# Performance work log

Measured on AMD Instinct MI355X. Metric: run time of the kernel, lower is better.

## Reference

```python
import jax, jax.numpy as jnp
import numpy as np


def setup_inputs() -> dict:
    key = jax.random.key(0)
    k1, k2, k3 = jax.random.split(key, 3)
    B, T, N = 256, 512, 128
    logits = jax.random.normal(k1, (B, T, N), dtype=jnp.float32)
    transitions = jax.random.normal(k2, (N, N), dtype=jnp.float32) * 0.1
    sequence_lengths = jax.random.randint(k3, (B,), 1, T + 1, dtype=jnp.int32)
    return {"logits": logits, "transitions": transitions,
            "sequence_lengths": sequence_lengths}


def reference(logits, transitions, sequence_lengths):
    # Viterbi decode (tfa.text.crf.crf_decode) + sequence mask, as in CRF.call.
    B, T, N = logits.shape
    state0 = logits[:, 0, :]                                  # [B,N]
    xs = jnp.moveaxis(logits[:, 1:, :], 1, 0)                 # [T-1,B,N]
    # step i (time t=i+1) is active iff t < seq_len
    active = jnp.arange(1, T)[:, None] < sequence_lengths[None, :]  # [T-1,B]

    def fwd_step(state, inp):
        x_t, act = inp
        # max-plus update: scores[b,i,j] = state[b,i] + transitions[i,j]
        scores = state[:, :, None] + transitions[None, :, :]  # [B,N,N]
        bp = jnp.argmax(scores, axis=1).astype(jnp.int32)     # [B,N]
        new_state = jnp.max(scores, axis=1) + x_t             # [B,N]
        # freeze state past the end of each sequence
        state = jnp.where(act[:, None], new_state, state)
        return state, bp

    final_state, bps = jax.lax.scan(fwd_step, state0, (xs, active))
    last_tag = jnp.argmax(final_state, axis=-1).astype(jnp.int32)  # [B]

    def bwd_step(cur, inp):
        bp_t, act = inp
        new = jnp.take_along_axis(bp_t, cur[:, None], axis=1)[:, 0]
        cur = jnp.where(act, new, cur)
        return cur, cur

    # reverse scan: ys[t] = decoded tag at time t, for t = 0..T-2
    _, tags = jax.lax.scan(bwd_step, last_tag, (bps, active), reverse=True)
    pred_ids = jnp.concatenate([jnp.moveaxis(tags, 0, 1),
                                last_tag[:, None]], axis=1)   # [B,T]
    mask = (jnp.arange(T)[None, :] < sequence_lengths[:, None]).astype(pred_ids.dtype)
    return pred_ids * mask
```

## Files before the change

kernel.cpp:

```cpp
#include <hip/hip_runtime.h>

#define TT 512
#define NN 128
#define NTHR 512
#define SROW 160
#define SW(i) (20 * ((i) >> 4) + ((i) & 15))
#define TTS 130
#define BD  64
#define MAXG 8

#define STEP_BARRIER() asm volatile("s_waitcnt lgkmcnt(0)\n\ts_barrier" ::: "memory")

template <int CTRL>
__device__ __forceinline__ int dpp_i(int x) {
    return __builtin_amdgcn_update_dpp(x, x, CTRL, 0xf, 0xf, true);
}
template <int CTRL>
__device__ __forceinline__ float dpp_f(float x) {
    union { float f; int i; } u; u.f = x;
    u.i = dpp_i<CTRL>(u.i);
    return u.f;
}
#define DPP_XOR1 0xB1
#define DPP_XOR2 0x4E
#define DPP_MIR7 0x141

__global__ __launch_bounds__(NTHR, 1)
void crf_viterbi_fast(const float* __restrict__ logits,
                      const float* __restrict__ trans,
                      const int* __restrict__ seqlen,
                      int* __restrict__ out,
                      float* __restrict__ ws) {
    __shared__ float stateBuf[2][SROW];
    __shared__ float tt[NN * TTS];
    __shared__ float redV[NN];
    __shared__ int   redI[NN];
    __shared__ int   tagBuf[TT];

    const int tid = threadIdx.x;
    const int j   = tid >> 3;
    const int c   = tid & 7;
    const int i0  = c << 4;
    const int b   = blockIdx.x;
    const int L   = seqlen[b];
    const int lm1 = L - 1;
    const int jx  = j + ((c & 1) << 6);

    const float* lrow = logits + (size_t)b * TT * NN;
    float* wsb = ws + (size_t)b * TT * NN;

    auto xl = [&](int r) -> float {
        r = (r < lm1) ? r : lm1;
        return lrow[r * NN + jx];
    };
    float X0 = xl(1), X1 = xl(2), X2 = xl(3), X3 = xl(4);

    float tr0[16], tr1[16];
    #pragma unroll
    for (int k = 0; k < 16; ++k) {
        tr0[k] = trans[(i0 + k) * NN + j];
        tr1[k] = trans[(i0 + k) * NN + j + 64];
    }

    #pragma unroll
    for (int k = 0; k < (NN * NN) / NTHR; ++k) {
        int idx = k * NTHR + tid;
        tt[(idx & 127) * TTS + (idx >> 7)] = trans[idx];
    }

    if (c < 2) {
        stateBuf[0][SW(jx)] = lrow[jx];
        wsb[jx] = 0.0f;
    }
    __syncthreads();

    #define TAGMAX(TR, OUT)                                                    \
    {                                                                          \
        float c0=a0.x+TR[0], c1=a0.y+TR[1], c2=a0.z+TR[2],  c3=a0.w+TR[3];     \
        float c4=a1.x+TR[4], c5=a1.y+TR[5], c6=a1.z+TR[6],  c7=a1.w+TR[7];     \
        float c8=a2.x+TR[8], c9=a2.y+TR[9], c10=a2.z+TR[10],c11=a2.w+TR[11];   \
        float c12=a3.x+TR[12],c13=a3.y+TR[13],c14=a3.z+TR[14],c15=a3.w+TR[15]; \
        float t0=fmaxf(fmaxf(c0,c1),c2),  t1=fmaxf(fmaxf(c3,c4),c5);           \
        float t2=fmaxf(fmaxf(c6,c7),c8),  t3=fmaxf(fmaxf(c9,c10),c11);         \
        float t4=fmaxf(fmaxf(c12,c13),c14);                                    \
        OUT = fmaxf(fmaxf(fmaxf(t0,t1),t2), fmaxf(fmaxf(t3,t4),c15));          \
    }

    auto vstep = [&](const float* st, float* dst, int t, float& xslot) {
        float xa_use = xslot;
        int tn = t + 4;
        tn = (tn < lm1) ? tn : lm1;
        xslot = lrow[tn * NN + jx];

        const float* sp = st + 20 * c;
        float4 a0 = *(const float4*)(sp);
        float4 a1 = *(const float4*)(sp + 4);
        float4 a2 = *(const float4*)(sp + 8);
        float4 a3 = *(const float4*)(sp + 12);

        float bv0, bv1;
        TAGMAX(tr0, bv0)
        TAGMAX(tr1, bv1)

        bv0 = fmaxf(bv0, dpp_f<DPP_XOR1>(bv0)); bv1 = fmaxf(bv1, dpp_f<DPP_XOR1>(bv1));
        bv0 = fmaxf(bv0, dpp_f<DPP_XOR2>(bv0)); bv1 = fmaxf(bv1, dpp_f<DPP_XOR2>(bv1));
        bv0 = fmaxf(bv0, dpp_f<DPP_MIR7>(bv0)); bv1 = fmaxf(bv1, dpp_f<DPP_MIR7>(bv1));

        if (c < 2) {
            float bv = c ? bv1 : bv0;
            dst[SW(jx)] = bv + xa_use;
            wsb[t * NN + jx] = bv;
        }
        STEP_BARRIER();
    };
    #undef TAGMAX

    int t = 1;
    for (; t + 4 < L; t += 4) {
        vstep(stateBuf[0], stateBuf[1], t,     X0);
        vstep(stateBuf[1], stateBuf[0], t + 1, X1);
        vstep(stateBuf[0], stateBuf[1], t + 2, X2);
        vstep(stateBuf[1], stateBuf[0], t + 3, X3);
    }
    if (t     < L) vstep(stateBuf[0], stateBuf[1], t,     X0);
    if (t + 1 < L) vstep(stateBuf[1], stateBuf[0], t + 1, X1);
    if (t + 2 < L) vstep(stateBuf[0], stateBuf[1], t + 2, X2);
    if (t + 3 < L) vstep(stateBuf[1], stateBuf[0], t + 3, X3);

    __syncthreads();
    const int pf = (L - 1) & 1;

    if (tid < NN) { redV[tid] = stateBuf[pf][SW(tid)]; redI[tid] = tid; }
    __syncthreads();
    #pragma unroll
    for (int off = 64; off >= 1; off >>= 1) {
        if (tid < off) {
            float va = redV[tid], vb = redV[tid + off];
            int   ia = redI[tid], ib = redI[tid + off];
            if (vb > va || (vb == va && ib < ia)) { redV[tid] = vb; redI[tid] = ib; }
        }
        __syncthreads();
    }

    if (tid < 64) {
        const int lane = tid;
        int jc = redI[0];
        if (lane == 0) tagBuf[L - 1] = jc;

        auto wrow = [&](int r) -> float2 {
            r = (r < 0) ? 0 : r;
            return *(const float2*)(wsb + r * NN + 2 * lane);
        };
        auto xrow = [&](int r) -> float2 {
            r = (r < 0) ? 0 : r;
            return *(const float2*)(lrow + r * NN + 2 * lane);
        };
        auto extract2 = [&](float2 v, int idx) -> float {
            int sel = idx >> 1;
            int wx = __builtin_amdgcn_readlane(__float_as_int(v.x), sel);
            int wy = __builtin_amdgcn_readlane(__float_as_int(v.y), sel);
            return __int_as_float((idx & 1) ? wy : wx);
        };

        float target;
        {
            float2 rT = wrow(L - 1);
            target = extract2(rT, jc);
        }

        auto chase = [&](float2 m, float2 xr, int tc) {
            float2 tp = *(const float2*)(tt + jc * TTS + 2 * lane);
            float cA = (m.x + xr.x) + tp.x;
            float cB = (m.y + xr.y) + tp.y;
            unsigned long long mA = __ballot(cA == target);
            unsigned long long mB = __ballot(cB == target);
            int iA = mA ? (2 * (__ffsll(mA) - 1))     : (1 << 30);
            int iB = mB ? (2 * (__ffsll(mB) - 1) + 1) : (1 << 30);
            int bp = (iA < iB) ? iA : iB;
            if (lane == 0) tagBuf[tc - 1] = bp;
            target = extract2(m, bp);
            jc = bp;
        };

        float2 m0 = wrow(L - 2), x0 = xrow(L - 2);
        float2 m1 = wrow(L - 3), x1 = xrow(L - 3);
        float2 m2 = wrow(L - 4), x2 = xrow(L - 4);
        float2 m3 = wrow(L - 5), x3 = xrow(L - 5);
        float2 m4 = wrow(L - 6), x4 = xrow(L - 6);
        float2 m5 = wrow(L - 7), x5 = xrow(L - 7);
        float2 m6 = wrow(L - 8), x6 = xrow(L - 8);
        float2 m7 = wrow(L - 9), x7 = xrow(L - 9);
        int tb = L - 1;
        while (tb >= 8) {
            chase(m0, x0, tb);     m0 = wrow(tb - 9);  x0 = xrow(tb - 9);
            chase(m1, x1, tb - 1); m1 = wrow(tb - 10); x1 = xrow(tb - 10);
            chase(m2, x2, tb - 2); m2 = wrow(tb - 11); x2 = xrow(tb - 11);
            chase(m3, x3, tb - 3); m3 = wrow(tb - 12); x3 = xrow(tb - 12);
            chase(m4, x4, tb - 4); m4 = wrow(tb - 13); x4 = xrow(tb - 13);
            chase(m5, x5, tb - 5); m5 = wrow(tb - 14); x5 = xrow(tb - 14);
            chase(m6, x6, tb - 6); m6 = wrow(tb - 15); x6 = xrow(tb - 15);
            chase(m7, x7, tb - 7); m7 = wrow(tb - 16); x7 = xrow(tb - 16);
            tb -= 8;
        }
        if (tb >= 1) chase(m0, x0, tb);
        if (tb >= 2) chase(m1, x1, tb - 1);
        if (tb >= 3) chase(m2, x2, tb - 2);
        if (tb >= 4) chase(m3, x3, tb - 3);
        if (tb >= 5) chase(m4, x4, tb - 4);
        if (tb >= 6) chase(m5, x5, tb - 5);
        if (tb >= 7) chase(m6, x6, tb - 6);
    }
    __syncthreads();

    out[(size_t)b * TT + tid] = (tid < L) ? tagBuf[tid] : 0;
}

__global__ __launch_bounds__(NTHR, 1)
void crf_viterbi_fallback(const float* __restrict__ logits,
                          const float* __restrict__ trans,
                          const int* __restrict__ seqlen,
                          int* __restrict__ out) {
    __shared__ float stateBuf[2][SROW];
    __shared__ float redV[NN];
    __shared__ int   redI[NN];
    __shared__ int   tagBuf[TT];
    __shared__ int   entryTag[MAXG];
    __shared__ unsigned char bp[TT][NN];
    __shared__ unsigned char hist[MAXG][BD][NN];

    const int tid = threadIdx.x;
    const int j   = tid >> 3;
    const int c   = tid & 7;
    const int i0  = c << 4;
    const int b   = blockIdx.x;
    const int L   = seqlen[b];

    float tr0[16], tr1[16];
    #pragma unroll
    for (int k = 0; k < 16; ++k) {
        tr0[k] = trans[(i0 + k) * NN + j];
        tr1[k] = trans[(i0 + k) * NN + j + 64];
    }

    const float* lrow = logits + (size_t)b * TT * NN;
    if (c < 2) {
        int jj = j + (c << 6);
        stateBuf[0][SW(jj)] = lrow[jj];
    }
    __syncthreads();

    float xa0 = lrow[NN + j], xa1 = lrow[NN + j + 64];
    int p = 0;
    for (int t = 1; t < L; ++t) {
        int tn = (t + 1 < L) ? (t + 1) : (L - 1);
        const float* lp = lrow + tn * NN;
        float xb0 = lp[j];
        float xb1 = lp[j + 64];

        const float* st = stateBuf[p] + 20 * c;
        float4 a0 = *(const float4*)(st);
        float4 a1 = *(const float4*)(st + 4);
        float4 a2 = *(const float4*)(st + 8);
        float4 a3 = *(const float4*)(st + 12);

        float best0 = -__builtin_inff(), best1 = -__builtin_inff();
        int arg0 = 0, arg1 = 0;
        #define ELEM(S, K)                                                  \
        {                                                                   \
            float sc = (S) + tr0[K];                                        \
            bool g = sc > best0; best0 = g ? sc : best0; arg0 = g ? (K) : arg0; \
            float sd = (S) + tr1[K];                                        \
            bool h = sd > best1; best1 = h ? sd : best1; arg1 = h ? (K) : arg1; \
        }
        ELEM(a0.x, 0)  ELEM(a0.y, 1)  ELEM(a0.z, 2)  ELEM(a0.w, 3)
        ELEM(a1.x, 4)  ELEM(a1.y, 5)  ELEM(a1.z, 6)  ELEM(a1.w, 7)
        ELEM(a2.x, 8)  ELEM(a2.y, 9)  ELEM(a2.z, 10) ELEM(a2.w, 11)
        ELEM(a3.x, 12) ELEM(a3.y, 13) ELEM(a3.z, 14) ELEM(a3.w, 15)
        #undef ELEM

        float bv0 = best0, bv1 = best1;
        int   bi0 = i0 + arg0, bi1 = i0 + arg1;
        #define MERGE_STAGE(CTRL, LOWER)                                   \
        {                                                                  \
            float p0 = dpp_f<CTRL>(bv0); int q0 = dpp_i<CTRL>(bi0);        \
            float p1 = dpp_f<CTRL>(bv1); int q1 = dpp_i<CTRL>(bi1);        \
            bool lower = (LOWER);                                          \
            bool t0 = (p0 > bv0) || (p0 == bv0 && lower);                  \
            bool t1 = (p1 > bv1) || (p1 == bv1 && lower);                  \
            bv0 = t0 ? p0 : bv0; bi0 = t0 ? q0 : bi0;                      \
            bv1 = t1 ? p1 : bv1; bi1 = t1 ? q1 : bi1;                      \
        }
        MERGE_STAGE(DPP_XOR1, (c & 1) != 0)
        MERGE_STAGE(DPP_XOR2, (c & 2) != 0)
        MERGE_STAGE(DPP_MIR7, (c & 4) != 0)
        #undef MERGE_STAGE

        if (c < 2) {
            int   jj = j + (c << 6);
            float bv = c ? bv1 : bv0;
            int   bi = c ? bi1 : bi0;
            float xx = c ? xa1 : xa0;
            stateBuf[p ^ 1][SW(jj)] = bv + xx;
            bp[t][jj] = (unsigned char)bi;
        }
        xa0 = xb0; xa1 = xb1;
        __syncthreads();
        p ^= 1;
    }

    if (tid < NN) { redV[tid] = stateBuf[p][SW(tid)]; redI[tid] = tid; }
    __syncthreads();
    #pragma unroll
    for (int off = 64; off >= 1; off >>= 1) {
        if (tid < off) {
            float va = redV[tid], vb = redV[tid + off];
            int   ia = redI[tid], ib = redI[tid + off];
            if (vb > va || (vb == va && ib < ia)) { redV[tid] = vb; redI[tid] = ib; }
        }
        __syncthreads();
    }

    const int M = L - 1;
    const int G = (M + BD - 1) / BD;
    {
        int s  = tid & 127;
        int gA = tid >> 7;
        int gB = gA + 4;
        int thA = M - gA * BD, thB = M - gB * BD;
        int dA  = (gA < G) ? ((thA < BD) ? thA : BD) : 0;
        int dB  = (gB < G) ? ((thB < BD) ? thB : BD) : 0;
        int curA = s, curB = s;
        int maxd = (dA > dB) ? dA : dB;
        for (int d = 0; d < maxd; ++d) {
            if (d < dA) { curA = bp[thA - d][curA]; hist[gA][d][s] = (unsigned char)curA; }
            if (d < dB) { curB = bp[thB - d][curB]; hist[gB][d][s] = (unsigned char)curB; }
        }
    }
    __syncthreads();
    if (tid == 0) {
        int e = redI[0];
        tagBuf[L - 1] = e;
        for (int g = 0; g < G; ++g) {
            entryTag[g] = e;
            if (g + 1 < G) e = hist[g][BD - 1][e];
        }
    }
    __syncthreads();
    {
        int g = tid >> 6, d = tid & 63;
        if (g < MAXG && g < G) {
            int th  = M - g * BD;
            int dep = (th < BD) ? th : BD;
            if (d < dep) {
                int e = entryTag[g];
                tagBuf[th - 1 - d] = hist[g][d][e];
            }
        }
    }
    __syncthreads();
    out[(size_t)b * TT + tid] = (tid < L) ? tagBuf[tid] : 0;
}

extern "C" void kernel_launch(void* const* d_in, const int* in_sizes, int n_in,
                              void* d_out, int out_size, void* d_ws, size_t ws_size,
                              hipStream_t stream) {
    const float* logits = (const float*)d_in[0];
    const float* trans  = (const float*)d_in[1];
    const int*   seqlen = (const int*)d_in[2];
    int*         out    = (int*)d_out;
    const int B = in_sizes[2];
    const size_t need = (size_t)B * TT * NN * sizeof(float);
    if (ws_size >= need) {
        crf_viterbi_fast<<<B, NTHR, 0, stream>>>(logits, trans, seqlen, out,
                                                 (float*)d_ws);
    } else {
        crf_viterbi_fallback<<<B, NTHR, 0, stream>>>(logits, trans, seqlen, out);
    }
}
```

Baseline: 313.6 us.

## Store uint8 backpointers in LDS and use parallel block traceback

The forward pass now computes each step's argmax with an equality search against the max, reduced with DPP min, and writes byte backpointers into shared memory. This replaces spilling max values to a global workspace and re-deriving argmaxes in a serial wave-level chase during traceback. The backward pass reuses the fallback kernel's chunked history-composition traceback, and the adds use packed float2 vectors. In exchange, every forward step does extra compare and DPP work and the kernel uses much more LDS.

```diff
diff --git a/kernel.cpp b/kernel.cpp
--- a/kernel.cpp
+++ b/kernel.cpp
@@ -5,11 +5,12 @@
 #define NTHR 512
 #define SROW 160
 #define SW(i) (20 * ((i) >> 4) + ((i) & 15))
-#define TTS 130
 #define BD  64
 #define MAXG 8
 
 #define STEP_BARRIER() asm volatile("s_waitcnt lgkmcnt(0)\n\ts_barrier" ::: "memory")
+
+typedef float v2f __attribute__((ext_vector_type(2)));
 
 template <int CTRL>
 __device__ __forceinline__ int dpp_i(int x) {
@@ -26,16 +27,17 @@
 #define DPP_MIR7 0x141
 
 __global__ __launch_bounds__(NTHR, 1)
-void crf_viterbi_fast(const float* __restrict__ logits,
-                      const float* __restrict__ trans,
-                      const int* __restrict__ seqlen,
-                      int* __restrict__ out,
-                      float* __restrict__ ws) {
+void crf_viterbi(const float* __restrict__ logits,
+                 const float* __restrict__ trans,
+                 const int* __restrict__ seqlen,
+                 int* __restrict__ out) {
     __shared__ float stateBuf[2][SROW];
-    __shared__ float tt[NN * TTS];
     __shared__ float redV[NN];
     __shared__ int   redI[NN];
     __shared__ int   tagBuf[TT];
+    __shared__ int   entryTag[MAXG];
+    __shared__ unsigned char bp[TT][NN];
+    __shared__ unsigned char hist[MAXG][BD][NN];
 
     const int tid = threadIdx.x;
     const int j   = tid >> 3;
@@ -47,7 +49,6 @@
     const int jx  = j + ((c & 1) << 6);
 
     const float* lrow = logits + (size_t)b * TT * NN;
-    float* wsb = ws + (size_t)b * TT * NN;
 
     auto xl = [&](int r) -> float {
         r = (r < lm1) ? r : lm1;
@@ -55,36 +56,17 @@
     };
     float X0 = xl(1), X1 = xl(2), X2 = xl(3), X3 = xl(4);
 
-    float tr0[16], tr1[16];
+    v2f tr0[8], tr1[8];
     #pragma unroll
-    for (int k = 0; k < 16; ++k) {
-        tr0[k] = trans[(i0 + k) * NN + j];
-        tr1[k] = trans[(i0 + k) * NN + j + 64];
-    }
-
-    #pragma unroll
-    for (int k = 0; k < (NN * NN) / NTHR; ++k) {
-        int idx = k * NTHR + tid;
-        tt[(idx & 127) * TTS + (idx >> 7)] = trans[idx];
-    }
-
-    if (c < 2) {
-        stateBuf[0][SW(jx)] = lrow[jx];
-        wsb[jx] = 0.0f;
-    }
-    __syncthreads();
-
-    #define TAGMAX(TR, OUT)                                                    \
-    {                                                                          \
-        float c0=a0.x+TR[0], c1=a0.y+TR[1], c2=a0.z+TR[2],  c3=a0.w+TR[3];     \
-        float c4=a1.x+TR[4], c5=a1.y+TR[5], c6=a1.z+TR[6],  c7=a1.w+TR[7];     \
-        float c8=a2.x+TR[8], c9=a2.y+TR[9], c10=a2.z+TR[10],c11=a2.w+TR[11];   \
-        float c12=a3.x+TR[12],c13=a3.y+TR[13],c14=a3.z+TR[14],c15=a3.w+TR[15]; \
-        float t0=fmaxf(fmaxf(c0,c1),c2),  t1=fmaxf(fmaxf(c3,c4),c5);           \
-        float t2=fmaxf(fmaxf(c6,c7),c8),  t3=fmaxf(fmaxf(c9,c10),c11);         \
-        float t4=fmaxf(fmaxf(c12,c13),c14);                                    \
-        OUT = fmaxf(fmaxf(fmaxf(t0,t1),t2), fmaxf(fmaxf(t3,t4),c15));          \
-    }
+    for (int p = 0; p < 8; ++p) {
+        tr0[p].x = trans[(i0 + 2 * p)     * NN + j];
+        tr0[p].y = trans[(i0 + 2 * p + 1) * NN + j];
+        tr1[p].x = trans[(i0 + 2 * p)     * NN + j + 64];
+        tr1[p].y = trans[(i0 + 2 * p + 1) * NN + j + 64];
+    }
+
+    if (c < 2) stateBuf[0][SW(jx)] = lrow[jx];
+    __syncthreads();
 
     auto vstep = [&](const float* st, float* dst, int t, float& xslot) {
         float xa_use = xslot;
@@ -98,9 +80,34 @@
         float4 a2 = *(const float4*)(sp + 8);
         float4 a3 = *(const float4*)(sp + 12);
 
+        v2f sv0 = {a0.x, a0.y}, sv1 = {a0.z, a0.w};
+        v2f sv2 = {a1.x, a1.y}, sv3 = {a1.z, a1.w};
+        v2f sv4 = {a2.x, a2.y}, sv5 = {a2.z, a2.w};
+        v2f sv6 = {a3.x, a3.y}, sv7 = {a3.z, a3.w};
+
+        v2f cc0[8], cc1[8];
+        cc0[0] = sv0 + tr0[0]; cc1[0] = sv0 + tr1[0];
+        cc0[1] = sv1 + tr0[1]; cc1[1] = sv1 + tr1[1];
+        cc0[2] = sv2 + tr0[2]; cc1[2] = sv2 + tr1[2];
+        cc0[3] = sv3 + tr0[3]; cc1[3] = sv3 + tr1[3];
+        cc0[4] = sv4 + tr0[4]; cc1[4] = sv4 + tr1[4];
+        cc0[5] = sv5 + tr0[5]; cc1[5] = sv5 + tr1[5];
+        cc0[6] = sv6 + tr0[6]; cc1[6] = sv6 + tr1[6];
+        cc0[7] = sv7 + tr0[7]; cc1[7] = sv7 + tr1[7];
+
+        #define TREE(CC, OUT)                                                  \
+        {                                                                      \
+            float t0 = fmaxf(fmaxf(CC[0].x, CC[0].y), CC[1].x);                \
+            float t1 = fmaxf(fmaxf(CC[1].y, CC[2].x), CC[2].y);                \
+            float t2 = fmaxf(fmaxf(CC[3].x, CC[3].y), CC[4].x);                \
+            float t3 = fmaxf(fmaxf(CC[4].y, CC[5].x), CC[5].y);                \
+            float t4 = fmaxf(fmaxf(CC[6].x, CC[6].y), CC[7].x);                \
+            OUT = fmaxf(fmaxf(fmaxf(t0, t1), t2), fmaxf(fmaxf(t3, t4), CC[7].y)); \
+        }
         float bv0, bv1;
-        TAGMAX(tr0, bv0)
-        TAGMAX(tr1, bv1)
+        TREE(cc0, bv0)
+        TREE(cc1, bv1)
+        #undef TREE
 
         bv0 = fmaxf(bv0, dpp_f<DPP_XOR1>(bv0)); bv1 = fmaxf(bv1, dpp_f<DPP_XOR1>(bv1));
         bv0 = fmaxf(bv0, dpp_f<DPP_XOR2>(bv0)); bv1 = fmaxf(bv1, dpp_f<DPP_XOR2>(bv1));
@@ -109,11 +116,26 @@
         if (c < 2) {
             float bv = c ? bv1 : bv0;
             dst[SW(jx)] = bv + xa_use;
-            wsb[t * NN + jx] = bv;
-        }
+        }
+
+        int idx0 = 255, idx1 = 255;
+        #pragma unroll
+        for (int k = 7; k >= 0; --k) {
+            if (cc0[k].y == bv0) idx0 = 2 * k + 1;
+            if (cc1[k].y == bv1) idx1 = 2 * k + 1;
+            if (cc0[k].x == bv0) idx0 = 2 * k;
+            if (cc1[k].x == bv1) idx1 = 2 * k;
+        }
+        int v0 = i0 + idx0;
+        int v1 = i0 + idx1;
+        v0 = min(v0, dpp_i<DPP_XOR1>(v0)); v1 = min(v1, dpp_i<DPP_XOR1>(v1));
+        v0 = min(v0, dpp_i<DPP_XOR2>(v0)); v1 = min(v1, dpp_i<DPP_XOR2>(v1));
+        v0 = min(v0, dpp_i<DPP_MIR7>(v0)); v1 = min(v1, dpp_i<DPP_MIR7>(v1));
+
+        if (c < 2) bp[t][jx] = (unsigned char)(c ? v1 : v0);
+
         STEP_BARRIER();
     };
-    #undef TAGMAX
 
     int t = 1;
     for (; t + 4 < L; t += 4) {
@@ -131,184 +153,6 @@
     const int pf = (L - 1) & 1;
 
     if (tid < NN) { redV[tid] = stateBuf[pf][SW(tid)]; redI[tid] = tid; }
-    __syncthreads();
-    #pragma unroll
-    for (int off = 64; off >= 1; off >>= 1) {
-        if (tid < off) {
-            float va = redV[tid], vb = redV[tid + off];
-            int   ia = redI[tid], ib = redI[tid + off];
-            if (vb > va || (vb == va && ib < ia)) { redV[tid] = vb; redI[tid] = ib; }
-        }
-        __syncthreads();
-    }
-
-    if (tid < 64) {
-        const int lane = tid;
-        int jc = redI[0];
-        if (lane == 0) tagBuf[L - 1] = jc;
-
-        auto wrow = [&](int r) -> float2 {
-            r = (r < 0) ? 0 : r;
-            return *(const float2*)(wsb + r * NN + 2 * lane);
-        };
-        auto xrow = [&](int r) -> float2 {
-            r = (r < 0) ? 0 : r;
-            return *(const float2*)(lrow + r * NN + 2 * lane);
-        };
-        auto extract2 = [&](float2 v, int idx) -> float {
-            int sel = idx >> 1;
-            int wx = __builtin_amdgcn_readlane(__float_as_int(v.x), sel);
-            int wy = __builtin_amdgcn_readlane(__float_as_int(v.y), sel);
-            return __int_as_float((idx & 1) ? wy : wx);
-        };
-
-        float target;
-        {
-            float2 rT = wrow(L - 1);
-            target = extract2(rT, jc);
-        }
-
-        auto chase = [&](float2 m, float2 xr, int tc) {
-            float2 tp = *(const float2*)(tt + jc * TTS + 2 * lane);
-            float cA = (m.x + xr.x) + tp.x;
-            float cB = (m.y + xr.y) + tp.y;
-            unsigned long long mA = __ballot(cA == target);
-            unsigned long long mB = __ballot(cB == target);
-            int iA = mA ? (2 * (__ffsll(mA) - 1))     : (1 << 30);
-            int iB = mB ? (2 * (__ffsll(mB) - 1) + 1) : (1 << 30);
-            int bp = (iA < iB) ? iA : iB;
-            if (lane == 0) tagBuf[tc - 1] = bp;
-            target = extract2(m, bp);
-            jc = bp;
-        };
-
-        float2 m0 = wrow(L - 2), x0 = xrow(L - 2);
-        float2 m1 = wrow(L - 3), x1 = xrow(L - 3);
-        float2 m2 = wrow(L - 4), x2 = xrow(L - 4);
-        float2 m3 = wrow(L - 5), x3 = xrow(L - 5);
-        float2 m4 = wrow(L - 6), x4 = xrow(L - 6);
-        float2 m5 = wrow(L - 7), x5 = xrow(L - 7);
-        float2 m6 = wrow(L - 8), x6 = xrow(L - 8);
-        float2 m7 = wrow(L - 9), x7 = xrow(L - 9);
-        int tb = L - 1;
-        while (tb >= 8) {
-            chase(m0, x0, tb);     m0 = wrow(tb - 9);  x0 = xrow(tb - 9);
-            chase(m1, x1, tb - 1); m1 = wrow(tb - 10); x1 = xrow(tb - 10);
-            chase(m2, x2, tb - 2); m2 = wrow(tb - 11); x2 = xrow(tb - 11);
-            chase(m3, x3, tb - 3); m3 = wrow(tb - 12); x3 = xrow(tb - 12);
-            chase(m4, x4, tb - 4); m4 = wrow(tb - 13); x4 = xrow(tb - 13);
-            chase(m5, x5, tb - 5); m5 = wrow(tb - 14); x5 = xrow(tb - 14);
-            chase(m6, x6, tb - 6); m6 = wrow(tb - 15); x6 = xrow(tb - 15);
-            chase(m7, x7, tb - 7); m7 = wrow(tb - 16); x7 = xrow(tb - 16);
-            tb -= 8;
-        }
-        if (tb >= 1) chase(m0, x0, tb);
-        if (tb >= 2) chase(m1, x1, tb - 1);
-        if (tb >= 3) chase(m2, x2, tb - 2);
-        if (tb >= 4) chase(m3, x3, tb - 3);
-        if (tb >= 5) chase(m4, x4, tb - 4);
-        if (tb >= 6) chase(m5, x5, tb - 5);
-        if (tb >= 7) chase(m6, x6, tb - 6);
-    }
-    __syncthreads();
-
-    out[(size_t)b * TT + tid] = (tid < L) ? tagBuf[tid] : 0;
-}
-
-__global__ __launch_bounds__(NTHR, 1)
-void crf_viterbi_fallback(const float* __restrict__ logits,
-                          const float* __restrict__ trans,
-                          const int* __restrict__ seqlen,
-                          int* __restrict__ out) {
-    __shared__ float stateBuf[2][SROW];
-    __shared__ float redV[NN];
-    __shared__ int   redI[NN];
-    __shared__ int   tagBuf[TT];
-    __shared__ int   entryTag[MAXG];
-    __shared__ unsigned char bp[TT][NN];
-    __shared__ unsigned char hist[MAXG][BD][NN];
-
-    const int tid = threadIdx.x;
-    const int j   = tid >> 3;
-    const int c   = tid & 7;
-    const int i0  = c << 4;
-    const int b   = blockIdx.x;
-    const int L   = seqlen[b];
-
-    float tr0[16], tr1[16];
-    #pragma unroll
-    for (int k = 0; k < 16; ++k) {
-        tr0[k] = trans[(i0 + k) * NN + j];
-        tr1[k] = trans[(i0 + k) * NN + j + 64];
-    }
-
-    const float* lrow = logits + (size_t)b * TT * NN;
-    if (c < 2) {
-        int jj = j + (c << 6);
-        stateBuf[0][SW(jj)] = lrow[jj];
-    }
-    __syncthreads();
-
-    float xa0 = lrow[NN + j], xa1 = lrow[NN + j + 64];
-    int p = 0;
-    for (int t = 1; t < L; ++t) {
-        int tn = (t + 1 < L) ? (t + 1) : (L - 1);
-        const float* lp = lrow + tn * NN;
-        float xb0 = lp[j];
-        float xb1 = lp[j + 64];
-
-        const float* st = stateBuf[p] + 20 * c;
-        float4 a0 = *(const float4*)(st);
-        float4 a1 = *(const float4*)(st + 4);
-        float4 a2 = *(const float4*)(st + 8);
-        float4 a3 = *(const float4*)(st + 12);
-
-        float best0 = -__builtin_inff(), best1 = -__builtin_inff();
-        int arg0 = 0, arg1 = 0;
-        #define ELEM(S, K)                                                  \
-        {                                                                   \
-            float sc = (S) + tr0[K];                                        \
-            bool g = sc > best0; best0 = g ? sc : best0; arg0 = g ? (K) : arg0; \
-            float sd = (S) + tr1[K];                                        \
-            bool h = sd > best1; best1 = h ? sd : best1; arg1 = h ? (K) : arg1; \
-        }
-        ELEM(a0.x, 0)  ELEM(a0.y, 1)  ELEM(a0.z, 2)  ELEM(a0.w, 3)
-        ELEM(a1.x, 4)  ELEM(a1.y, 5)  ELEM(a1.z, 6)  ELEM(a1.w, 7)
-        ELEM(a2.x, 8)  ELEM(a2.y, 9)  ELEM(a2.z, 10) ELEM(a2.w, 11)
-        ELEM(a3.x, 12) ELEM(a3.y, 13) ELEM(a3.z, 14) ELEM(a3.w, 15)
-        #undef ELEM
-
-        float bv0 = best0, bv1 = best1;
-        int   bi0 = i0 + arg0, bi1 = i0 + arg1;
-        #define MERGE_STAGE(CTRL, LOWER)                                   \
-        {                                                                  \
-            float p0 = dpp_f<CTRL>(bv0); int q0 = dpp_i<CTRL>(bi0);        \
-            float p1 = dpp_f<CTRL>(bv1); int q1 = dpp_i<CTRL>(bi1);        \
-            bool lower = (LOWER);                                          \
-            bool t0 = (p0 > bv0) || (p0 == bv0 && lower);                  \
-            bool t1 = (p1 > bv1) || (p1 == bv1 && lower);                  \
-            bv0 = t0 ? p0 : bv0; bi0 = t0 ? q0 : bi0;                      \
-            bv1 = t1 ? p1 : bv1; bi1 = t1 ? q1 : bi1;                      \
-        }
-        MERGE_STAGE(DPP_XOR1, (c & 1) != 0)
-        MERGE_STAGE(DPP_XOR2, (c & 2) != 0)
-        MERGE_STAGE(DPP_MIR7, (c & 4) != 0)
-        #undef MERGE_STAGE
-
-        if (c < 2) {
-            int   jj = j + (c << 6);
-            float bv = c ? bv1 : bv0;
-            int   bi = c ? bi1 : bi0;
-            float xx = c ? xa1 : xa0;
-            stateBuf[p ^ 1][SW(jj)] = bv + xx;
-            bp[t][jj] = (unsigned char)bi;
-        }
-        xa0 = xb0; xa1 = xb1;
-        __syncthreads();
-        p ^= 1;
-    }
-
-    if (tid < NN) { redV[tid] = stateBuf[p][SW(tid)]; redI[tid] = tid; }
     __syncthreads();
     #pragma unroll
     for (int off = 64; off >= 1; off >>= 1) {
@@ -358,6 +202,7 @@
         }
     }
     __syncthreads();
+
     out[(size_t)b * TT + tid] = (tid < L) ? tagBuf[tid] : 0;
 }
 
@@ -369,11 +214,6 @@
     const int*   seqlen = (const int*)d_in[2];
     int*         out    = (int*)d_out;
     const int B = in_sizes[2];
-    const size_t need = (size_t)B * TT * NN * sizeof(float);
-    if (ws_size >= need) {
-        crf_viterbi_fast<<<B, NTHR, 0, stream>>>(logits, trans, seqlen, out,
-                                                 (float*)d_ws);
-    } else {
-        crf_viterbi_fallback<<<B, NTHR, 0, stream>>>(logits, trans, seqlen, out);
-    }
-}
+    (void)d_ws; (void)ws_size;
+    crf_viterbi<<<B, NTHR, 0, stream>>>(logits, trans, seqlen, out);
+}
```

New measurement: 420.2 us. 1.34x slower.

## Halve fast-kernel threads, give each lane 32 states with packed v2f max-plus

Applied to the files above, without the earlier changes.

The fast Viterbi kernel now runs 256 threads instead of 512, so each output tag is reduced by 4 lanes over 32 predecessor states rather than 8 lanes over 16. The inner max-plus reduction is written with 2-wide float vectors so the compiler can emit packed FP32 adds, and one DPP shuffle stage is removed. The aim is to cut per-step barrier cost and cross-lane shuffle latency on the serial time recurrence. In exchange, each lane does twice as much arithmetic per step, needs more registers, and the epilogue writes two outputs per thread. The fallback kernel keeps 512 threads via a separate define.

```diff
diff --git a/kernel.cpp b/kernel.cpp
--- a/kernel.cpp
+++ b/kernel.cpp
@@ -2,7 +2,8 @@
 
 #define TT 512
 #define NN 128
-#define NTHR 512
+#define NTHR 256
+#define FTHR 512
 #define SROW 160
 #define SW(i) (20 * ((i) >> 4) + ((i) & 15))
 #define TTS 130
@@ -10,6 +11,11 @@
 #define MAXG 8
 
 #define STEP_BARRIER() asm volatile("s_waitcnt lgkmcnt(0)\n\ts_barrier" ::: "memory")
+
+typedef float v2f __attribute__((ext_vector_type(2)));
+__device__ __forceinline__ v2f vmax2(v2f a, v2f b) {
+    v2f r; r.x = fmaxf(a.x, b.x); r.y = fmaxf(a.y, b.y); return r;
+}
 
 template <int CTRL>
 __device__ __forceinline__ int dpp_i(int x) {
@@ -38,9 +44,9 @@
     __shared__ int   tagBuf[TT];
 
     const int tid = threadIdx.x;
-    const int j   = tid >> 3;
-    const int c   = tid & 7;
-    const int i0  = c << 4;
+    const int j   = tid >> 2;
+    const int c   = tid & 3;
+    const int i0  = c << 5;
     const int b   = blockIdx.x;
     const int L   = seqlen[b];
     const int lm1 = L - 1;
@@ -55,14 +61,15 @@
     };
     float X0 = xl(1), X1 = xl(2), X2 = xl(3), X3 = xl(4);
 
-    float tr0[16], tr1[16];
+    v2f tr0[16], tr1[16];
     #pragma unroll
-    for (int k = 0; k < 16; ++k) {
-        tr0[k] = trans[(i0 + k) * NN + j];
-        tr1[k] = trans[(i0 + k) * NN + j + 64];
-    }
-
-    #pragma unroll
+    for (int p = 0; p < 16; ++p) {
+        tr0[p].x = trans[(i0 + 2 * p)     * NN + j];
+        tr0[p].y = trans[(i0 + 2 * p + 1) * NN + j];
+        tr1[p].x = trans[(i0 + 2 * p)     * NN + j + 64];
+        tr1[p].y = trans[(i0 + 2 * p + 1) * NN + j + 64];
+    }
+
     for (int k = 0; k < (NN * NN) / NTHR; ++k) {
         int idx = k * NTHR + tid;
         tt[(idx & 127) * TTS + (idx >> 7)] = trans[idx];
@@ -74,16 +81,21 @@
     }
     __syncthreads();
 
-    #define TAGMAX(TR, OUT)                                                    \
+    #define REDUCE32(TR, OUT)                                                  \
     {                                                                          \
-        float c0=a0.x+TR[0], c1=a0.y+TR[1], c2=a0.z+TR[2],  c3=a0.w+TR[3];     \
-        float c4=a1.x+TR[4], c5=a1.y+TR[5], c6=a1.z+TR[6],  c7=a1.w+TR[7];     \
-        float c8=a2.x+TR[8], c9=a2.y+TR[9], c10=a2.z+TR[10],c11=a2.w+TR[11];   \
-        float c12=a3.x+TR[12],c13=a3.y+TR[13],c14=a3.z+TR[14],c15=a3.w+TR[15]; \
-        float t0=fmaxf(fmaxf(c0,c1),c2),  t1=fmaxf(fmaxf(c3,c4),c5);           \
-        float t2=fmaxf(fmaxf(c6,c7),c8),  t3=fmaxf(fmaxf(c9,c10),c11);         \
-        float t4=fmaxf(fmaxf(c12,c13),c14);                                    \
-        OUT = fmaxf(fmaxf(fmaxf(t0,t1),t2), fmaxf(fmaxf(t3,t4),c15));          \
+        v2f m0 = vmax2(sv0 + TR[0],  sv1 + TR[1]);                             \
+        v2f m1 = vmax2(sv2 + TR[2],  sv3 + TR[3]);                             \
+        v2f m2 = vmax2(sv4 + TR[4],  sv5 + TR[5]);                             \
+        v2f m3 = vmax2(sv6 + TR[6],  sv7 + TR[7]);                             \
+        v2f m4 = vmax2(sv8 + TR[8],  sv9 + TR[9]);                             \
+        v2f m5 = vmax2(sv10 + TR[10], sv11 + TR[11]);                          \
+        v2f m6 = vmax2(sv12 + TR[12], sv13 + TR[13]);                          \
+        v2f m7 = vmax2(sv14 + TR[14], sv15 + TR[15]);                          \
+        m0 = vmax2(m0, m1); m2 = vmax2(m2, m3);                                \
+        m4 = vmax2(m4, m5); m6 = vmax2(m6, m7);                                \
+        m0 = vmax2(m0, m2); m4 = vmax2(m4, m6);                                \
+        m0 = vmax2(m0, m4);                                                    \
+        OUT = fmaxf(m0.x, m0.y);                                               \
     }
 
     auto vstep = [&](const float* st, float* dst, int t, float& xslot) {
@@ -92,19 +104,31 @@
         tn = (tn < lm1) ? tn : lm1;
         xslot = lrow[tn * NN + jx];
 
-        const float* sp = st + 20 * c;
+        const float* sp = st + 40 * c;
         float4 a0 = *(const float4*)(sp);
         float4 a1 = *(const float4*)(sp + 4);
         float4 a2 = *(const float4*)(sp + 8);
         float4 a3 = *(const float4*)(sp + 12);
+        float4 a4 = *(const float4*)(sp + 20);
+        float4 a5 = *(const float4*)(sp + 24);
+        float4 a6 = *(const float4*)(sp + 28);
+        float4 a7 = *(const float4*)(sp + 32);
+
+        v2f sv0  = {a0.x, a0.y}, sv1  = {a0.z, a0.w};
+        v2f sv2  = {a1.x, a1.y}, sv3  = {a1.z, a1.w};
+        v2f sv4  = {a2.x, a2.y}, sv5  = {a2.z, a2.w};
+        v2f sv6  = {a3.x, a3.y}, sv7  = {a3.z, a3.w};
+        v2f sv8  = {a4.x, a4.y}, sv9  = {a4.z, a4.w};
+        v2f sv10 = {a5.x, a5.y}, sv11 = {a5.z, a5.w};
+        v2f sv12 = {a6.x, a6.y}, sv13 = {a6.z, a6.w};
+        v2f sv14 = {a7.x, a7.y}, sv15 = {a7.z, a7.w};
 
         float bv0, bv1;
-        TAGMAX(tr0, bv0)
-        TAGMAX(tr1, bv1)
+        REDUCE32(tr0, bv0)
+        REDUCE32(tr1, bv1)
 
         bv0 = fmaxf(bv0, dpp_f<DPP_XOR1>(bv0)); bv1 = fmaxf(bv1, dpp_f<DPP_XOR1>(bv1));
         bv0 = fmaxf(bv0, dpp_f<DPP_XOR2>(bv0)); bv1 = fmaxf(bv1, dpp_f<DPP_XOR2>(bv1));
-        bv0 = fmaxf(bv0, dpp_f<DPP_MIR7>(bv0)); bv1 = fmaxf(bv1, dpp_f<DPP_MIR7>(bv1));
 
         if (c < 2) {
             float bv = c ? bv1 : bv0;
@@ -113,7 +137,7 @@
         }
         STEP_BARRIER();
     };
-    #undef TAGMAX
+    #undef REDUCE32
 
     int t = 1;
     for (; t + 4 < L; t += 4) {
@@ -212,10 +236,11 @@
     }
     __syncthreads();
 
-    out[(size_t)b * TT + tid] = (tid < L) ? tagBuf[tid] : 0;
-}
-
-__global__ __launch_bounds__(NTHR, 1)
+    out[(size_t)b * TT + tid]       = (tid < L)       ? tagBuf[tid]       : 0;
+    out[(size_t)b * TT + tid + 256] = (tid + 256 < L) ? tagBuf[tid + 256] : 0;
+}
+
+__global__ __launch_bounds__(FTHR, 1)
 void crf_viterbi_fallback(const float* __restrict__ logits,
                           const float* __restrict__ trans,
                           const int* __restrict__ seqlen,
@@ -374,6 +399,6 @@
         crf_viterbi_fast<<<B, NTHR, 0, stream>>>(logits, trans, seqlen, out,
                                                  (float*)d_ws);
     } else {
-        crf_viterbi_fallback<<<B, NTHR, 0, stream>>>(logits, trans, seqlen, out);
-    }
-}
+        crf_viterbi_fallback<<<B, FTHR, 0, stream>>>(logits, trans, seqlen, out);
+    }
+}
```

Result: no change. 312.3 us, median of 2 (-0.4%).

## Halve forward-pass threads with 8 outputs per 16-lane group and packed v2f math

Applied to the files above, without the earlier changes.

The fast Viterbi kernel now uses 256 threads instead of 512. Each 16-lane group computes 8 destination tags over an 8-element slice of the source states, using packed two-wide float adds and max, and adds a fourth DPP reduction stage across 16 lanes. Logits are prefetched and the new state and workspace row are written as float4 vectors. The aim is fewer waves taking part in each per-step barrier and more work per thread; in exchange each thread holds 64 transition values in registers and runs a longer DPP reduction chain.

```diff
diff --git a/kernel.cpp b/kernel.cpp
--- a/kernel.cpp
+++ b/kernel.cpp
@@ -2,14 +2,22 @@
 
 #define TT 512
 #define NN 128
-#define NTHR 512
-#define SROW 160
-#define SW(i) (20 * ((i) >> 4) + ((i) & 15))
+#define NTHR 256
+#define FTHR 512
+#define SROW 192
+#define SW(i) (12 * ((i) >> 3) + ((i) & 7))
+#define FSROW 160
+#define SWF(i) (20 * ((i) >> 4) + ((i) & 15))
 #define TTS 130
 #define BD  64
 #define MAXG 8
 
 #define STEP_BARRIER() asm volatile("s_waitcnt lgkmcnt(0)\n\ts_barrier" ::: "memory")
+
+typedef float v2f __attribute__((ext_vector_type(2)));
+__device__ __forceinline__ v2f vmax2(v2f a, v2f b) {
+    v2f r; r.x = fmaxf(a.x, b.x); r.y = fmaxf(a.y, b.y); return r;
+}
 
 template <int CTRL>
 __device__ __forceinline__ int dpp_i(int x) {
@@ -21,9 +29,10 @@
     u.i = dpp_i<CTRL>(u.i);
     return u.f;
 }
-#define DPP_XOR1 0xB1
-#define DPP_XOR2 0x4E
-#define DPP_MIR7 0x141
+#define DPP_XOR1  0xB1
+#define DPP_XOR2  0x4E
+#define DPP_MIR7  0x141
+#define DPP_MIR15 0x140
 
 __global__ __launch_bounds__(NTHR, 1)
 void crf_viterbi_fast(const float* __restrict__ logits,
@@ -37,83 +46,97 @@
     __shared__ int   redI[NN];
     __shared__ int   tagBuf[TT];
 
-    const int tid = threadIdx.x;
-    const int j   = tid >> 3;
-    const int c   = tid & 7;
-    const int i0  = c << 4;
-    const int b   = blockIdx.x;
-    const int L   = seqlen[b];
-    const int lm1 = L - 1;
-    const int jx  = j + ((c & 1) << 6);
+    const int tid  = threadIdx.x;
+    const int wave = tid >> 6;
+    const int lane = tid & 63;
+    const int g    = lane >> 4;
+    const int c    = lane & 15;
+    const int jb   = wave * 32 + g * 8;
+    const int b    = blockIdx.x;
+    const int L    = seqlen[b];
+    const int lm1  = L - 1;
 
     const float* lrow = logits + (size_t)b * TT * NN;
     float* wsb = ws + (size_t)b * TT * NN;
 
-    auto xl = [&](int r) -> float {
+    struct X8 { float4 a, b; };
+    auto xl = [&](int r) -> X8 {
         r = (r < lm1) ? r : lm1;
-        return lrow[r * NN + jx];
+        X8 v;
+        v.a = *(const float4*)(lrow + r * NN + jb);
+        v.b = *(const float4*)(lrow + r * NN + jb + 4);
+        return v;
     };
-    float X0 = xl(1), X1 = xl(2), X2 = xl(3), X3 = xl(4);
-
-    float tr0[16], tr1[16];
+    X8 X0 = xl(1), X1 = xl(2), X2 = xl(3), X3 = xl(4);
+
+    v2f tr[8][4];
     #pragma unroll
-    for (int k = 0; k < 16; ++k) {
-        tr0[k] = trans[(i0 + k) * NN + j];
-        tr1[k] = trans[(i0 + k) * NN + j + 64];
-    }
-
-    #pragma unroll
+    for (int u = 0; u < 8; ++u)
+        #pragma unroll
+        for (int q = 0; q < 4; ++q) {
+            tr[u][q].x = trans[(8 * c + 2 * q)     * NN + jb + u];
+            tr[u][q].y = trans[(8 * c + 2 * q + 1) * NN + jb + u];
+        }
+
     for (int k = 0; k < (NN * NN) / NTHR; ++k) {
         int idx = k * NTHR + tid;
         tt[(idx & 127) * TTS + (idx >> 7)] = trans[idx];
     }
 
-    if (c < 2) {
-        stateBuf[0][SW(jx)] = lrow[jx];
-        wsb[jx] = 0.0f;
-    }
-    __syncthreads();
-
-    #define TAGMAX(TR, OUT)                                                    \
-    {                                                                          \
-        float c0=a0.x+TR[0], c1=a0.y+TR[1], c2=a0.z+TR[2],  c3=a0.w+TR[3];     \
-        float c4=a1.x+TR[4], c5=a1.y+TR[5], c6=a1.z+TR[6],  c7=a1.w+TR[7];     \
-        float c8=a2.x+TR[8], c9=a2.y+TR[9], c10=a2.z+TR[10],c11=a2.w+TR[11];   \
-        float c12=a3.x+TR[12],c13=a3.y+TR[13],c14=a3.z+TR[14],c15=a3.w+TR[15]; \
-        float t0=fmaxf(fmaxf(c0,c1),c2),  t1=fmaxf(fmaxf(c3,c4),c5);           \
-        float t2=fmaxf(fmaxf(c6,c7),c8),  t3=fmaxf(fmaxf(c9,c10),c11);         \
-        float t4=fmaxf(fmaxf(c12,c13),c14);                                    \
-        OUT = fmaxf(fmaxf(fmaxf(t0,t1),t2), fmaxf(fmaxf(t3,t4),c15));          \
-    }
-
-    auto vstep = [&](const float* st, float* dst, int t, float& xslot) {
-        float xa_use = xslot;
+    if (tid < NN) {
+        stateBuf[0][SW(tid)] = lrow[tid];
+        wsb[tid] = 0.0f;
+    }
+    __syncthreads();
+
+    auto vstep = [&](const float* st, float* dst, int t, X8& xslot) {
+        X8 xa = xslot;
         int tn = t + 4;
         tn = (tn < lm1) ? tn : lm1;
-        xslot = lrow[tn * NN + jx];
-
-        const float* sp = st + 20 * c;
+        xslot.a = *(const float4*)(lrow + tn * NN + jb);
+        xslot.b = *(const float4*)(lrow + tn * NN + jb + 4);
+
+        const float* sp = st + 12 * c;
         float4 a0 = *(const float4*)(sp);
         float4 a1 = *(const float4*)(sp + 4);
-        float4 a2 = *(const float4*)(sp + 8);
-        float4 a3 = *(const float4*)(sp + 12);
-
-        float bv0, bv1;
-        TAGMAX(tr0, bv0)
-        TAGMAX(tr1, bv1)
-
-        bv0 = fmaxf(bv0, dpp_f<DPP_XOR1>(bv0)); bv1 = fmaxf(bv1, dpp_f<DPP_XOR1>(bv1));
-        bv0 = fmaxf(bv0, dpp_f<DPP_XOR2>(bv0)); bv1 = fmaxf(bv1, dpp_f<DPP_XOR2>(bv1));
-        bv0 = fmaxf(bv0, dpp_f<DPP_MIR7>(bv0)); bv1 = fmaxf(bv1, dpp_f<DPP_MIR7>(bv1));
-
-        if (c < 2) {
-            float bv = c ? bv1 : bv0;
-            dst[SW(jx)] = bv + xa_use;
-            wsb[t * NN + jx] = bv;
+        v2f sv0 = {a0.x, a0.y}, sv1 = {a0.z, a0.w};
+        v2f sv2 = {a1.x, a1.y}, sv3 = {a1.z, a1.w};
+
+        float bv[8];
+        #pragma unroll
+        for (int u = 0; u < 8; ++u) {
+            v2f c0 = sv0 + tr[u][0];
+            v2f c1 = sv1 + tr[u][1];
+            v2f c2 = sv2 + tr[u][2];
+            v2f c3 = sv3 + tr[u][3];
+            v2f m  = vmax2(vmax2(c0, c1), vmax2(c2, c3));
+            bv[u]  = fmaxf(m.x, m.y);
+        }
+
+        #pragma unroll
+        for (int u = 0; u < 8; ++u) bv[u] = fmaxf(bv[u], dpp_f<DPP_XOR1>(bv[u]));
+        #pragma unroll
+        for (int u = 0; u < 8; ++u) bv[u] = fmaxf(bv[u], dpp_f<DPP_XOR2>(bv[u]));
+        #pragma unroll
+        for (int u = 0; u < 8; ++u) bv[u] = fmaxf(bv[u], dpp_f<DPP_MIR7>(bv[u]));
+        #pragma unroll
+        for (int u = 0; u < 8; ++u) bv[u] = fmaxf(bv[u], dpp_f<DPP_MIR15>(bv[u]));
+
+        if (c == 0) {
+            float4 w0 = {bv[0] + xa.a.x, bv[1] + xa.a.y,
+                         bv[2] + xa.a.z, bv[3] + xa.a.w};
+            float4 w1 = {bv[4] + xa.b.x, bv[5] + xa.b.y,
+                         bv[6] + xa.b.z, bv[7] + xa.b.w};
+            float* dp = dst + SW(jb);
+            *(float4*)(dp)     = w0;
+            *(float4*)(dp + 4) = w1;
+            float4 m0 = {bv[0], bv[1], bv[2], bv[3]};
+            float4 m1 = {bv[4], bv[5], bv[6], bv[7]};
+            *(float4*)(wsb + t * NN + jb)     = m0;
+            *(float4*)(wsb + t * NN + jb + 4) = m1;
         }
         STEP_BARRIER();
     };
-    #undef TAGMAX
 
     int t = 1;
     for (; t + 4 < L; t += 4) {
@@ -143,17 +166,17 @@
     }
 
     if (tid < 64) {
-        const int lane = tid;
+        const int ln = tid;
         int jc = redI[0];
-        if (lane == 0) tagBuf[L - 1] = jc;
+        if (ln == 0) tagBuf[L - 1] = jc;
 
         auto wrow = [&](int r) -> float2 {
             r = (r < 0) ? 0 : r;
-            return *(const float2*)(wsb + r * NN + 2 * lane);
+            return *(const float2*)(wsb + r * NN + 2 * ln);
         };
         auto xrow = [&](int r) -> float2 {
             r = (r < 0) ? 0 : r;
-            return *(const float2*)(lrow + r * NN + 2 * lane);
+            return *(const float2*)(lrow + r * NN + 2 * ln);
         };
         auto extract2 = [&](float2 v, int idx) -> float {
             int sel = idx >> 1;
@@ -169,7 +192,7 @@
         }
 
         auto chase = [&](float2 m, float2 xr, int tc) {
-            float2 tp = *(const float2*)(tt + jc * TTS + 2 * lane);
+            float2 tp = *(const float2*)(tt + jc * TTS + 2 * ln);
             float cA = (m.x + xr.x) + tp.x;
             float cB = (m.y + xr.y) + tp.y;
             unsigned long long mA = __ballot(cA == target);
@@ -177,7 +200,7 @@
             int iA = mA ? (2 * (__ffsll(mA) - 1))     : (1 << 30);
             int iB = mB ? (2 * (__ffsll(mB) - 1) + 1) : (1 << 30);
             int bp = (iA < iB) ? iA : iB;
-            if (lane == 0) tagBuf[tc - 1] = bp;
+            if (ln == 0) tagBuf[tc - 1] = bp;
             target = extract2(m, bp);
             jc = bp;
         };
@@ -212,15 +235,16 @@
     }
     __syncthreads();
 
-    out[(size_t)b * TT + tid] = (tid < L) ? tagBuf[tid] : 0;
-}
-
-__global__ __launch_bounds__(NTHR, 1)
+    out[(size_t)b * TT + tid]       = (tid < L)       ? tagBuf[tid]       : 0;
+    out[(size_t)b * TT + tid + 256] = (tid + 256 < L) ? tagBuf[tid + 256] : 0;
+}
+
+__global__ __launch_bounds__(FTHR, 1)
 void crf_viterbi_fallback(const float* __restrict__ logits,
                           const float* __restrict__ trans,
                           const int* __restrict__ seqlen,
                           int* __restrict__ out) {
-    __shared__ float stateBuf[2][SROW];
+    __shared__ float stateBuf[2][FSROW];
     __shared__ float redV[NN];
     __shared__ int   redI[NN];
     __shared__ int   tagBuf[TT];
@@ -245,7 +269,7 @@
     const float* lrow = logits + (size_t)b * TT * NN;
     if (c < 2) {
         int jj = j + (c << 6);
-        stateBuf[0][SW(jj)] = lrow[jj];
+        stateBuf[0][SWF(jj)] = lrow[jj];
     }
     __syncthreads();
 
@@ -300,7 +324,7 @@
             float bv = c ? bv1 : bv0;
             int   bi = c ? bi1 : bi0;
             float xx = c ? xa1 : xa0;
-            stateBuf[p ^ 1][SW(jj)] = bv + xx;
+            stateBuf[p ^ 1][SWF(jj)] = bv + xx;
             bp[t][jj] = (unsigned char)bi;
         }
         xa0 = xb0; xa1 = xb1;
@@ -308,7 +332,7 @@
         p ^= 1;
     }
 
-    if (tid < NN) { redV[tid] = stateBuf[p][SW(tid)]; redI[tid] = tid; }
+    if (tid < NN) { redV[tid] = stateBuf[p][SWF(tid)]; redI[tid] = tid; }
     __syncthreads();
     #pragma unroll
     for (int off = 64; off >= 1; off >>= 1) {
@@ -374,6 +398,6 @@
         crf_viterbi_fast<<<B, NTHR, 0, stream>>>(logits, trans, seqlen, out,
                                                  (float*)d_ws);
     } else {
-        crf_viterbi_fallback<<<B, NTHR, 0, stream>>>(logits, trans, seqlen, out);
-    }
-}
+        crf_viterbi_fallback<<<B, FTHR, 0, stream>>>(logits, trans, seqlen, out);
+    }
+}
```

Result: slower. 403.7 us (+28.7%).
